# Kernel optimization log

Measured on AMD Instinct MI355X. Metric: run time of the kernel, lower is better.

The kernel has to match this reference:

```python
import jax, jax.numpy as jnp
import numpy as np

B, S, D, H = 2, 2048, 1024, 16
HD = D // H  # head_dim = 64
SCALE = 1.0 / np.sqrt(np.float32(D))  # original divides by sqrt(d_keys) == sqrt(d_model)


def setup_inputs() -> dict:
    key = jax.random.key(0)
    ks = jax.random.split(key, 8)
    inp = {
        "query": jax.random.normal(ks[0], (B, S, D), jnp.float32),
        "key": jax.random.normal(ks[1], (B, S, D), jnp.float32),
        "value": jax.random.normal(ks[2], (B, S, D), jnp.float32),
        # nn.Linear weights stored as [out, in]; y = x @ W.T
        "Wq": jax.random.normal(ks[3], (D, D), jnp.float32) * 0.02,
        "Wk": jax.random.normal(ks[4], (D, D), jnp.float32) * 0.02,
        "Wv": jax.random.normal(ks[5], (D, D), jnp.float32) * 0.02,
        "Wo": jax.random.normal(ks[6], (D, D), jnp.float32) * 0.02,
        "bo": jax.random.normal(ks[7], (D,), jnp.float32) * 0.02,
    }
    return inp


def reference(query, key, value, Wq, Wk, Wv, Wo, bo):
    # projections (no bias)
    Q = jnp.einsum('bsd,ed->bse', query, Wq)
    K = jnp.einsum('bsd,ed->bse', key, Wk)
    V = jnp.einsum('bsd,ed->bse', value, Wv)
    # split heads -> [B, H, S, HD]
    Q = Q.reshape(B, S, H, HD).transpose(0, 2, 1, 3)
    K = K.reshape(B, S, H, HD).transpose(0, 2, 1, 3)
    V = V.reshape(B, S, H, HD).transpose(0, 2, 1, 3)
    # scores [B,H,S,S]; note: scaled by 1/sqrt(d_model), matching the source
    scores = jnp.einsum('bhqd,bhkd->bhqk', Q, K) * SCALE
    attn = jax.nn.softmax(scores, axis=-1)  # dropout_ratio=0 -> identity
    ctx = jnp.einsum('bhqk,bhkd->bhqd', attn, V)
    ctx = ctx.transpose(0, 2, 1, 3).reshape(B, S, D)
    return jnp.einsum('bsd,ed->bse', ctx, Wo) + bo
```

## Files before the change

### kernel.cpp

```cpp
#include <hip/hip_runtime.h>
#include <hip/hip_bf16.h>

#define B_  2
#define S_  2048
#define D_  1024
#define H_  16
#define HD_ 64
#define SCALE_ 0.03125f
#define LOG2E_ 1.4426950408889634f
#define QSCALE_ (SCALE_ * LOG2E_)

typedef __bf16 bf16;
typedef __attribute__((ext_vector_type(8))) __bf16 bf16x8;
typedef __attribute__((ext_vector_type(8))) unsigned short u16x8;
typedef __attribute__((ext_vector_type(4))) __bf16 bf16x4;
typedef __attribute__((ext_vector_type(4))) float f32x4;

__device__ __forceinline__ void gload_lds16(const void* g, void* l) {
  __builtin_amdgcn_global_load_lds(
      (const __attribute__((address_space(1))) unsigned int*)g,
      (__attribute__((address_space(3))) unsigned int*)l,
      16, 0, 0);
}

__device__ __forceinline__ bf16x8 load8(const float* p) {
  const float4 a = *(const float4*)p;
  const float4 b = *(const float4*)(p + 4);
  bf16x8 r;
  r[0] = (bf16)a.x; r[1] = (bf16)a.y; r[2] = (bf16)a.z; r[3] = (bf16)a.w;
  r[4] = (bf16)b.x; r[5] = (bf16)b.y; r[6] = (bf16)b.z; r[7] = (bf16)b.w;
  return r;
}
__device__ __forceinline__ bf16x8 load8(const bf16* p) {
  return *(const bf16x8*)p;
}

__global__ __launch_bounds__(256)
void wconv_kernel(const float* __restrict__ Wq, const float* __restrict__ Wk,
                  const float* __restrict__ Wv, const float* __restrict__ Wo,
                  bf16* __restrict__ dst)
{
  const int n4  = (blockIdx.x * 256 + threadIdx.x) * 4;
  const int m   = n4 >> 20;
  const int off = n4 & ((1 << 20) - 1);
  const float* src = m == 0 ? Wq : (m == 1 ? Wk : (m == 2 ? Wv : Wo));
  const float4 a = *(const float4*)(src + off);
  bf16x4 o = {(bf16)a.x, (bf16)a.y, (bf16)a.z, (bf16)a.w};
  *(bf16x4*)(dst + n4) = o;
}

__global__ __launch_bounds__(256)
void conv_kernel(const float* __restrict__ Wq, const float* __restrict__ Wk,
                 const float* __restrict__ Wv, const float* __restrict__ Wo,
                 const float* __restrict__ q, const float* __restrict__ k,
                 const float* __restrict__ v, bf16* __restrict__ dst)
{
  const size_t MI = (size_t)1 << 20;
  const size_t n4 = ((size_t)blockIdx.x * 256 + threadIdx.x) * 4;
  const float* src;
  size_t so, dof;
  if (n4 < 4 * MI) {
    const int m = (int)(n4 >> 20);
    src = m == 0 ? Wq : (m == 1 ? Wk : (m == 2 ? Wv : Wo));
    so  = n4 & (MI - 1);
    dof = n4;
  } else {
    const size_t a = n4 - 4 * MI;
    const int m = (int)(a >> 22);
    src = m == 0 ? q : (m == 1 ? k : v);
    so  = a & (4 * MI - 1);
    dof = n4 + 4 * MI;
  }
  const float4 a4 = *(const float4*)(src + so);
  bf16x4 o = {(bf16)a4.x, (bf16)a4.y, (bf16)a4.z, (bf16)a4.w};
  *(bf16x4*)(dst + dof) = o;
}

__global__ __launch_bounds__(256, 2)
void gemm_qkv3_kernel(const bf16* __restrict__ Ab, const bf16* __restrict__ Wb,
                      bf16* __restrict__ Cq, bf16* __restrict__ Ck,
                      bf16* __restrict__ Cv)
{
  __shared__ bf16 lA[128 * 32];
  __shared__ bf16 lB[128 * 32];

  const int sel = blockIdx.y >> 3;
  const int bn  = blockIdx.y & 7;
  const bf16* A  = Ab + ((size_t)sel << 22);
  const bf16* Bw = Wb + ((size_t)sel << 20);
  bf16*       C  = sel == 0 ? Cq : (sel == 1 ? Ck : Cv);
  const float scale = sel == 0 ? QSCALE_ : 1.0f;

  const int t    = threadIdx.x;
  const int wave = t >> 6;
  const int lane = t & 63;
  const int quad = lane >> 4;
  const int l16  = lane & 15;
  const int bm = blockIdx.x;
  const int wm = (wave >> 1) * 64;
  const int wn = (wave & 1) * 64;

  const int srow = t >> 2;
  const int scol = (t & 3) * 8;
  const bf16* gA = A  + (size_t)(bm * 128 + srow) * D_ + scol;
  const bf16* gB = Bw + (size_t)(bn * 128 + srow) * D_ + scol;

  f32x4 acc[4][4] = {};

  for (int k0 = 0; k0 < D_; k0 += 32) {
    __syncthreads();
    gload_lds16(gA,                   (char*)lA + wave * 1024);
    gload_lds16(gA + (size_t)64 * D_, (char*)lA + 4096 + wave * 1024);
    gload_lds16(gB,                   (char*)lB + wave * 1024);
    gload_lds16(gB + (size_t)64 * D_, (char*)lB + 4096 + wave * 1024);
    __syncthreads();

    bf16x8 af[4], bfr[4];
#pragma unroll
    for (int i = 0; i < 4; ++i) {
      af[i]  = *(const bf16x8*)(lA + (wm + i * 16 + l16) * 32 + quad * 8);
      bfr[i] = *(const bf16x8*)(lB + (wn + i * 16 + l16) * 32 + quad * 8);
    }
#pragma unroll
    for (int mi = 0; mi < 4; ++mi)
#pragma unroll
      for (int ni = 0; ni < 4; ++ni)
        acc[mi][ni] = __builtin_amdgcn_mfma_f32_16x16x32_bf16(
            af[mi], bfr[ni], acc[mi][ni], 0, 0, 0);

    gA += 32;
    gB += 32;
  }

#pragma unroll
  for (int mi = 0; mi < 4; ++mi) {
#pragma unroll
    for (int ni = 0; ni < 4; ++ni) {
      const int col = bn * 128 + wn + ni * 16 + l16;
#pragma unroll
      for (int r = 0; r < 4; ++r) {
        const int row = bm * 128 + wm + mi * 16 + quad * 4 + r;
        C[(size_t)row * D_ + col] = (bf16)(acc[mi][ni][r] * scale);
      }
    }
  }
}

__global__ __launch_bounds__(256, 2)
void gemm_qkv_b_kernel(const float* __restrict__ Aq, const float* __restrict__ Ak,
                       const float* __restrict__ Av, const bf16* __restrict__ Wb,
                       bf16* __restrict__ Cq, bf16* __restrict__ Ck,
                       bf16* __restrict__ Cv)
{
  __shared__ bf16 lA[128 * 32];
  __shared__ bf16 lB[128 * 32];

  const int sel = blockIdx.y >> 3;
  const int bn  = blockIdx.y & 7;
  const float* A  = sel == 0 ? Aq : (sel == 1 ? Ak : Av);
  const bf16*  Bw = Wb + ((size_t)sel << 20);
  bf16*        C  = sel == 0 ? Cq : (sel == 1 ? Ck : Cv);
  const float scale = sel == 0 ? QSCALE_ : 1.0f;

  const int t    = threadIdx.x;
  const int wave = t >> 6;
  const int lane = t & 63;
  const int quad = lane >> 4;
  const int l16  = lane & 15;
  const int bm = blockIdx.x;
  const int wm = (wave >> 1) * 64;
  const int wn = (wave & 1) * 64;

  const int srow = t >> 2;
  const int scol = (t & 3) * 8;
  const float* gA  = A  + (size_t)(bm * 128 + srow) * D_ + scol;
  const bf16*  gBb = Bw + (size_t)(bn * 128 + srow) * D_ + scol;

  f32x4 acc[4][4] = {};

  bf16x8 a0 = load8(gA);
  bf16x8 a1 = load8(gA + (size_t)64 * D_);

  for (int k0 = 0; k0 < D_; k0 += 32) {
    __syncthreads();
    *(bf16x8*)(lA + srow * 32 + scol)        = a0;
    *(bf16x8*)(lA + (srow + 64) * 32 + scol) = a1;
    gload_lds16(gBb,                   (char*)lB + wave * 1024);
    gload_lds16(gBb + (size_t)64 * D_, (char*)lB + 4096 + wave * 1024);
    gBb += 32;
    __syncthreads();

    if (k0 + 32 < D_) {
      gA += 32;
      a0 = load8(gA);
      a1 = load8(gA + (size_t)64 * D_);
    }

    bf16x8 af[4], bfr[4];
#pragma unroll
    for (int i = 0; i < 4; ++i) {
      af[i]  = *(const bf16x8*)(lA + (wm + i * 16 + l16) * 32 + quad * 8);
      bfr[i] = *(const bf16x8*)(lB + (wn + i * 16 + l16) * 32 + quad * 8);
    }
#pragma unroll
    for (int mi = 0; mi < 4; ++mi)
#pragma unroll
      for (int ni = 0; ni < 4; ++ni)
        acc[mi][ni] = __builtin_amdgcn_mfma_f32_16x16x32_bf16(
            af[mi], bfr[ni], acc[mi][ni], 0, 0, 0);
  }

#pragma unroll
  for (int mi = 0; mi < 4; ++mi) {
#pragma unroll
    for (int ni = 0; ni < 4; ++ni) {
      const int col = bn * 128 + wn + ni * 16 + l16;
#pragma unroll
      for (int r = 0; r < 4; ++r) {
        const int row = bm * 128 + wm + mi * 16 + quad * 4 + r;
        C[(size_t)row * D_ + col] = (bf16)(acc[mi][ni][r] * scale);
      }
    }
  }
}

__global__ __launch_bounds__(256, 2)
void gemm_out_b_kernel(const bf16* __restrict__ A, const bf16* __restrict__ Bw,
                       const float* __restrict__ bias, float* __restrict__ C)
{
  __shared__ bf16 lA[128 * 32];
  __shared__ bf16 lB[64 * 32];

  const int t    = threadIdx.x;
  const int wave = t >> 6;
  const int lane = t & 63;
  const int quad = lane >> 4;
  const int l16  = lane & 15;
  const int bm = blockIdx.x;
  const int bn = blockIdx.y;
  const int wm = wave * 32;

  const int srow = t >> 2;
  const int scol = (t & 3) * 8;
  const bf16* gA = A  + (size_t)(bm * 128 + srow) * D_ + scol;
  const bf16* gB = Bw + (size_t)(bn * 64 + srow) * D_ + scol;

  f32x4 acc[2][4] = {};

  for (int k0 = 0; k0 < D_; k0 += 32) {
    __syncthreads();
    gload_lds16(gA,                   (char*)lA + wave * 1024);
    gload_lds16(gA + (size_t)64 * D_, (char*)lA + 4096 + wave * 1024);
    gload_lds16(gB,                   (char*)lB + wave * 1024);
    __syncthreads();

    bf16x8 af[2], bfr[4];
#pragma unroll
    for (int i = 0; i < 2; ++i)
      af[i]  = *(const bf16x8*)(lA + (wm + i * 16 + l16) * 32 + quad * 8);
#pragma unroll
    for (int i = 0; i < 4; ++i)
      bfr[i] = *(const bf16x8*)(lB + (i * 16 + l16) * 32 + quad * 8);
#pragma unroll
    for (int mi = 0; mi < 2; ++mi)
#pragma unroll
      for (int ni = 0; ni < 4; ++ni)
        acc[mi][ni] = __builtin_amdgcn_mfma_f32_16x16x32_bf16(
            af[mi], bfr[ni], acc[mi][ni], 0, 0, 0);

    gA += 32;
    gB += 32;
  }

  float bv[4];
#pragma unroll
  for (int ni = 0; ni < 4; ++ni)
    bv[ni] = bias[bn * 64 + ni * 16 + l16];
#pragma unroll
  for (int mi = 0; mi < 2; ++mi) {
#pragma unroll
    for (int ni = 0; ni < 4; ++ni) {
      const int col = bn * 64 + ni * 16 + l16;
#pragma unroll
      for (int r = 0; r < 4; ++r) {
        const int row = bm * 128 + wm + mi * 16 + quad * 4 + r;
        C[(size_t)row * D_ + col] = acc[mi][ni][r] + bv[ni];
      }
    }
  }
}

__global__ __launch_bounds__(256, 2)
void gemm_qkv_kernel(const float* __restrict__ Aq, const float* __restrict__ Ak,
                     const float* __restrict__ Av, const float* __restrict__ Wq,
                     const float* __restrict__ Wk, const float* __restrict__ Wv,
                     bf16* __restrict__ Cq, bf16* __restrict__ Ck,
                     bf16* __restrict__ Cv)
{
  __shared__ bf16 lA[128 * 32];
  __shared__ bf16 lB[128 * 32];

  const int sel = blockIdx.y >> 3;
  const int bn  = blockIdx.y & 7;
  const float* A  = sel == 0 ? Aq : (sel == 1 ? Ak : Av);
  const float* Bw = sel == 0 ? Wq : (sel == 1 ? Wk : Wv);
  bf16*        C  = sel == 0 ? Cq : (sel == 1 ? Ck : Cv);
  const float scale = sel == 0 ? QSCALE_ : 1.0f;

  const int t    = threadIdx.x;
  const int wave = t >> 6;
  const int lane = t & 63;
  const int quad = lane >> 4;
  const int l16  = lane & 15;
  const int bm = blockIdx.x;
  const int wm = (wave >> 1) * 64;
  const int wn = (wave & 1) * 64;

  const int srow = t >> 2;
  const int scol = (t & 3) * 8;
  const float* gA = A  + (size_t)(bm * 128 + srow) * D_ + scol;
  const float* gB = Bw + (size_t)(bn * 128 + srow) * D_ + scol;

  f32x4 acc[4][4] = {};

  for (int k0 = 0; k0 < D_; k0 += 32) {
    const bf16x8 a0 = load8(gA);
    const bf16x8 a1 = load8(gA + (size_t)64 * D_);
    const bf16x8 b0 = load8(gB);
    const bf16x8 b1 = load8(gB + (size_t)64 * D_);

    __syncthreads();
    *(bf16x8*)(lA + srow * 32 + scol)        = a0;
    *(bf16x8*)(lA + (srow + 64) * 32 + scol) = a1;
    *(bf16x8*)(lB + srow * 32 + scol)        = b0;
    *(bf16x8*)(lB + (srow + 64) * 32 + scol) = b1;
    __syncthreads();

    bf16x8 af[4], bfr[4];
#pragma unroll
    for (int i = 0; i < 4; ++i) {
      af[i]  = *(const bf16x8*)(lA + (wm + i * 16 + l16) * 32 + quad * 8);
      bfr[i] = *(const bf16x8*)(lB + (wn + i * 16 + l16) * 32 + quad * 8);
    }
#pragma unroll
    for (int mi = 0; mi < 4; ++mi)
#pragma unroll
      for (int ni = 0; ni < 4; ++ni)
        acc[mi][ni] = __builtin_amdgcn_mfma_f32_16x16x32_bf16(
            af[mi], bfr[ni], acc[mi][ni], 0, 0, 0);

    gA += 32;
    gB += 32;
  }

#pragma unroll
  for (int mi = 0; mi < 4; ++mi) {
#pragma unroll
    for (int ni = 0; ni < 4; ++ni) {
      const int col = bn * 128 + wn + ni * 16 + l16;
#pragma unroll
      for (int r = 0; r < 4; ++r) {
        const int row = bm * 128 + wm + mi * 16 + quad * 4 + r;
        C[(size_t)row * D_ + col] = (bf16)(acc[mi][ni][r] * scale);
      }
    }
  }
}

__global__ __launch_bounds__(256, 2)
void gemm_out_kernel(const bf16* __restrict__ A, const float* __restrict__ Bw,
                     const float* __restrict__ bias, float* __restrict__ C)
{
  __shared__ bf16 lA[128 * 32];
  __shared__ bf16 lB[64 * 32];

  const int t    = threadIdx.x;
  const int wave = t >> 6;
  const int lane = t & 63;
  const int quad = lane >> 4;
  const int l16  = lane & 15;
  const int bm = blockIdx.x;
  const int bn = blockIdx.y;
  const int wm = wave * 32;

  const int srow = t >> 2;
  const int scol = (t & 3) * 8;
  const bf16*  gA = A  + (size_t)(bm * 128 + srow) * D_ + scol;
  const float* gB = Bw + (size_t)(bn * 64 + srow) * D_ + scol;

  f32x4 acc[2][4] = {};

  for (int k0 = 0; k0 < D_; k0 += 32) {
    const bf16x8 a0 = load8(gA);
    const bf16x8 a1 = load8(gA + (size_t)64 * D_);
    const bf16x8 b0 = load8(gB);

    __syncthreads();
    *(bf16x8*)(lA + srow * 32 + scol)        = a0;
    *(bf16x8*)(lA + (srow + 64) * 32 + scol) = a1;
    *(bf16x8*)(lB + srow * 32 + scol)        = b0;
    __syncthreads();

    bf16x8 af[2], bfr[4];
#pragma unroll
    for (int i = 0; i < 2; ++i)
      af[i]  = *(const bf16x8*)(lA + (wm + i * 16 + l16) * 32 + quad * 8);
#pragma unroll
    for (int i = 0; i < 4; ++i)
      bfr[i] = *(const bf16x8*)(lB + (i * 16 + l16) * 32 + quad * 8);
#pragma unroll
    for (int mi = 0; mi < 2; ++mi)
#pragma unroll
      for (int ni = 0; ni < 4; ++ni)
        acc[mi][ni] = __builtin_amdgcn_mfma_f32_16x16x32_bf16(
            af[mi], bfr[ni], acc[mi][ni], 0, 0, 0);

    gA += 32;
    gB += 32;
  }

  float bv[4];
#pragma unroll
  for (int ni = 0; ni < 4; ++ni)
    bv[ni] = bias[bn * 64 + ni * 16 + l16];
#pragma unroll
  for (int mi = 0; mi < 2; ++mi) {
#pragma unroll
    for (int ni = 0; ni < 4; ++ni) {
      const int col = bn * 64 + ni * 16 + l16;
#pragma unroll
      for (int r = 0; r < 4; ++r) {
        const int row = bm * 128 + wm + mi * 16 + quad * 4 + r;
        C[(size_t)row * D_ + col] = acc[mi][ni][r] + bv[ni];
      }
    }
  }
}

__global__ __launch_bounds__(256, 2)
void attn_kernel(const bf16* Q, const bf16* __restrict__ K,
                 const bf16* __restrict__ V, bf16* O)
{
  __shared__ bf16 lQ[128 * 72];
  __shared__ bf16 lK[64 * 72];
  __shared__ bf16 lVT[64 * 72];
  __shared__ bf16 lP[4][32 * 72];

  const int t    = threadIdx.x;
  const int wave = t >> 6;
  const int lane = t & 63;
  const int quad = lane >> 4;
  const int l16  = lane & 15;

  const int flat = blockIdx.y * 16 + blockIdx.x;
  const int qt   = (flat >> 3) & 15;
  const int bh   = (flat & 7) * 4 + (flat >> 7);
  const size_t headoff =
      (size_t)(bh >> 4) * ((size_t)S_ * D_) + (size_t)(bh & 15) * HD_;

  const int sr  = t >> 3;
  const int scx = (t & 7) * 8;
#pragma unroll
  for (int i = 0; i < 4; ++i) {
    const bf16x8 qv =
        *(const bf16x8*)(Q + headoff + (size_t)(qt * 128 + sr + 32 * i) * D_ + scx);
    *(bf16x8*)(lQ + (sr + 32 * i) * 72 + scx) = qv;
  }
  __syncthreads();

  bf16x8 qf[2][2];
#pragma unroll
  for (int m = 0; m < 2; ++m)
#pragma unroll
    for (int ks = 0; ks < 2; ++ks)
      qf[m][ks] = *(const bf16x8*)(lQ + (wave * 32 + m * 16 + l16) * 72 +
                                   (ks * 4 + quad) * 8);

  f32x4 acco[2][4] = {};
  float den[2] = {0.f, 0.f};

  const int dp = t & 31;
  const int kg = t >> 5;

  bf16x8 pk0, pk1;
  unsigned int pv[8];
  {
    const bf16* kb = K + headoff + (size_t)sr * D_ + scx;
    pk0 = load8(kb);
    pk1 = load8(kb + (size_t)32 * D_);
    const bf16* vb = V + headoff + (size_t)(kg * 8) * D_ + 2 * dp;
#pragma unroll
    for (int j = 0; j < 8; ++j)
      pv[j] = *(const unsigned int*)(vb + (size_t)j * D_);
  }

  for (int kt = 0; kt < S_ / 64; ++kt) {
    __syncthreads();

    *(bf16x8*)(lK + sr * 72 + scx)        = pk0;
    *(bf16x8*)(lK + (sr + 32) * 72 + scx) = pk1;
    {
      u16x8 w0, w1;
#pragma unroll
      for (int j = 0; j < 8; ++j) {
        w0[j] = (unsigned short)(pv[j] & 0xffffu);
        w1[j] = (unsigned short)(pv[j] >> 16);
      }
      *(u16x8*)(lVT + (2 * dp) * 72 + kg * 8)     = w0;
      *(u16x8*)(lVT + (2 * dp + 1) * 72 + kg * 8) = w1;
    }
    __syncthreads();

    if (kt + 1 < S_ / 64) {
      const bf16* kb = K + headoff + (size_t)((kt + 1) * 64 + sr) * D_ + scx;
      pk0 = load8(kb);
      pk1 = load8(kb + (size_t)32 * D_);
      const bf16* vb = V + headoff + (size_t)((kt + 1) * 64 + kg * 8) * D_ + 2 * dp;
#pragma unroll
      for (int j = 0; j < 8; ++j)
        pv[j] = *(const unsigned int*)(vb + (size_t)j * D_);
    }

    f32x4 sc[2][4] = {};
#pragma unroll
    for (int nt = 0; nt < 4; ++nt) {
#pragma unroll
      for (int ks = 0; ks < 2; ++ks) {
        const bf16x8 kf =
            *(const bf16x8*)(lK + (nt * 16 + l16) * 72 + (ks * 4 + quad) * 8);
#pragma unroll
        for (int m = 0; m < 2; ++m)
          sc[m][nt] = __builtin_amdgcn_mfma_f32_16x16x32_bf16(
              kf, qf[m][ks], sc[m][nt], 0, 0, 0);
      }
    }

    bf16* lPw = lP[wave];
#pragma unroll
    for (int m = 0; m < 2; ++m) {
#pragma unroll
      for (int nt = 0; nt < 4; ++nt) {
        bf16x4 pw;
#pragma unroll
        for (int r = 0; r < 4; ++r) {
          const float p = __builtin_amdgcn_exp2f(sc[m][nt][r]);
          pw[r] = (bf16)p;
          den[m] += p;
        }
        *(bf16x4*)(lPw + (m * 16 + l16) * 72 + nt * 16 + quad * 4) = pw;
      }
    }

    __syncthreads();

    bf16x8 pf[2][2];
#pragma unroll
    for (int m = 0; m < 2; ++m)
#pragma unroll
      for (int ks = 0; ks < 2; ++ks)
        pf[m][ks] = *(const bf16x8*)(lPw + (m * 16 + l16) * 72 +
                                     ks * 32 + quad * 8);
#pragma unroll
    for (int dt = 0; dt < 4; ++dt) {
#pragma unroll
      for (int ks = 0; ks < 2; ++ks) {
        const bf16x8 vf =
            *(const bf16x8*)(lVT + (dt * 16 + l16) * 72 + (ks * 4 + quad) * 8);
#pragma unroll
        for (int m = 0; m < 2; ++m)
          acco[m][dt] = __builtin_amdgcn_mfma_f32_16x16x32_bf16(
              pf[m][ks], vf, acco[m][dt], 0, 0, 0);
      }
    }
  }

#pragma unroll
  for (int m = 0; m < 2; ++m) {
    den[m] += __shfl_xor(den[m], 16);
    den[m] += __shfl_xor(den[m], 32);
  }
#pragma unroll
  for (int m = 0; m < 2; ++m) {
#pragma unroll
    for (int r = 0; r < 4; ++r) {
      const float rd  = 1.f / __shfl(den[m], quad * 4 + r);
      const int   row = qt * 128 + wave * 32 + m * 16 + quad * 4 + r;
#pragma unroll
      for (int dt = 0; dt < 4; ++dt)
        O[headoff + (size_t)row * D_ + dt * 16 + l16] =
            (bf16)(acco[m][dt][r] * rd);
    }
  }
}

extern "C" void kernel_launch(void* const* d_in, const int* in_sizes, int n_in,
                              void* d_out, int out_size, void* d_ws, size_t ws_size,
                              hipStream_t stream)
{
  const float* q  = (const float*)d_in[0];
  const float* k  = (const float*)d_in[1];
  const float* v  = (const float*)d_in[2];
  const float* Wq = (const float*)d_in[3];
  const float* Wk = (const float*)d_in[4];
  const float* Wv = (const float*)d_in[5];
  const float* Wo = (const float*)d_in[6];
  const float* bo = (const float*)d_in[7];
  float* outf = (float*)d_out;
  bf16*  outs = (bf16*)d_out;
  bf16*  wsb  = (bf16*)d_ws;

  const size_t MD = (size_t)B_ * S_ * D_;

  dim3 blk(256);
  dim3 gqkv(B_ * S_ / 128, 24);
  dim3 gattn(S_ / 128, B_ * H_);
  dim3 gout(B_ * S_ / 128, D_ / 64);

  bf16* Kp = outs;
  bf16* Vp = outs + MD;

  if (ws_size >= (size_t)40 << 20) {
    bf16* Wb = wsb;
    bf16* Qp = wsb + MD;
    bf16* Ab = wsb + 2 * MD;

    conv_kernel<<<16384, blk, 0, stream>>>(Wq, Wk, Wv, Wo, q, k, v, wsb);
    gemm_qkv3_kernel<<<gqkv, blk, 0, stream>>>(Ab, Wb, Qp, Kp, Vp);
    attn_kernel<<<gattn, blk, 0, stream>>>(Qp, Kp, Vp, Qp);
    gemm_out_b_kernel<<<gout, blk, 0, stream>>>(Qp, Wb + 3 * ((size_t)1 << 20),
                                                bo, outf);
  } else if (ws_size >= (size_t)16 << 20) {
    bf16* Wb = wsb;
    bf16* Qp = wsb + MD;

    wconv_kernel<<<4096, blk, 0, stream>>>(Wq, Wk, Wv, Wo, Wb);
    gemm_qkv_b_kernel<<<gqkv, blk, 0, stream>>>(q, k, v, Wb, Qp, Kp, Vp);
    attn_kernel<<<gattn, blk, 0, stream>>>(Qp, Kp, Vp, Qp);
    gemm_out_b_kernel<<<gout, blk, 0, stream>>>(Qp, Wb + 3 * ((size_t)1 << 20),
                                                bo, outf);
  } else {
    bf16* Qp = wsb;

    gemm_qkv_kernel<<<gqkv, blk, 0, stream>>>(q, k, v, Wq, Wk, Wv,
                                              Qp, Kp, Vp);
    attn_kernel<<<gattn, blk, 0, stream>>>(Qp, Kp, Vp, Qp);
    gemm_out_kernel<<<gout, blk, 0, stream>>>(Qp, Wo, bo, outf);
  }
}
```

Baseline: 211.5 us.

## Double-buffer K/V tiles in LDS and cut attention-loop barriers to one

The attention kernel now keeps two LDS buffers each for the K tile and the transposed V tile. Each iteration writes the next tile into the spare buffer while computing on the current one, and global prefetch now runs two tiles ahead. The barrier before the P·V stage becomes a compiler-only scheduling fence, because each wave reads only the P buffer it wrote itself. That leaves a single __syncthreads per iteration instead of three. The cost is more LDS per block and one extra prefetch stage held in registers, which could reduce occupancy.

New measurement: 213.1 us. Within noise of the previous version (+0.8%).

```diff
diff --git a/kernel.cpp b/kernel.cpp
--- a/kernel.cpp
+++ b/kernel.cpp
@@ -442,8 +442,8 @@
                  const bf16* __restrict__ V, bf16* O)
 {
   __shared__ bf16 lQ[128 * 72];
-  __shared__ bf16 lK[64 * 72];
-  __shared__ bf16 lVT[64 * 72];
+  __shared__ bf16 lK[2][64 * 72];
+  __shared__ bf16 lVT[2][64 * 72];
   __shared__ bf16 lP[4][32 * 72];
 
   const int t    = threadIdx.x;
@@ -458,6 +458,9 @@
   const size_t headoff =
       (size_t)(bh >> 4) * ((size_t)S_ * D_) + (size_t)(bh & 15) * HD_;
 
+  const bf16* Kb = K + headoff;
+  const bf16* Vb = V + headoff;
+
   const int sr  = t >> 3;
   const int scx = (t & 7) * 8;
 #pragma unroll
@@ -482,40 +485,67 @@
   const int dp = t & 31;
   const int kg = t >> 5;
 
+  const int NT = S_ / 64;
   bf16x8 pk0, pk1;
   unsigned int pv[8];
+
   {
-    const bf16* kb = K + headoff + (size_t)sr * D_ + scx;
+    const bf16* kb = Kb + (size_t)sr * D_ + scx;
     pk0 = load8(kb);
     pk1 = load8(kb + (size_t)32 * D_);
-    const bf16* vb = V + headoff + (size_t)(kg * 8) * D_ + 2 * dp;
+    const bf16* vb = Vb + (size_t)(kg * 8) * D_ + 2 * dp;
 #pragma unroll
     for (int j = 0; j < 8; ++j)
       pv[j] = *(const unsigned int*)(vb + (size_t)j * D_);
   }
-
-  for (int kt = 0; kt < S_ / 64; ++kt) {
-    __syncthreads();
-
-    *(bf16x8*)(lK + sr * 72 + scx)        = pk0;
-    *(bf16x8*)(lK + (sr + 32) * 72 + scx) = pk1;
-    {
+  {
+    *(bf16x8*)(lK[0] + sr * 72 + scx)        = pk0;
+    *(bf16x8*)(lK[0] + (sr + 32) * 72 + scx) = pk1;
+    u16x8 w0, w1;
+#pragma unroll
+    for (int j = 0; j < 8; ++j) {
+      w0[j] = (unsigned short)(pv[j] & 0xffffu);
+      w1[j] = (unsigned short)(pv[j] >> 16);
+    }
+    *(u16x8*)(lVT[0] + (2 * dp) * 72 + kg * 8)     = w0;
+    *(u16x8*)(lVT[0] + (2 * dp + 1) * 72 + kg * 8) = w1;
+  }
+  {
+    const bf16* kb = Kb + (size_t)(64 + sr) * D_ + scx;
+    pk0 = load8(kb);
+    pk1 = load8(kb + (size_t)32 * D_);
+    const bf16* vb = Vb + (size_t)(64 + kg * 8) * D_ + 2 * dp;
+#pragma unroll
+    for (int j = 0; j < 8; ++j)
+      pv[j] = *(const unsigned int*)(vb + (size_t)j * D_);
+  }
+  __syncthreads();
+
+  for (int kt = 0; kt < NT; ++kt) {
+    const int cur = kt & 1;
+    bf16* lKc  = lK[cur];
+    bf16* lVc  = lVT[cur];
+
+    if (kt + 1 < NT) {
+      bf16* lKn = lK[cur ^ 1];
+      bf16* lVn = lVT[cur ^ 1];
+      *(bf16x8*)(lKn + sr * 72 + scx)        = pk0;
+      *(bf16x8*)(lKn + (sr + 32) * 72 + scx) = pk1;
       u16x8 w0, w1;
 #pragma unroll
       for (int j = 0; j < 8; ++j) {
         w0[j] = (unsigned short)(pv[j] & 0xffffu);
         w1[j] = (unsigned short)(pv[j] >> 16);
       }
-      *(u16x8*)(lVT + (2 * dp) * 72 + kg * 8)     = w0;
-      *(u16x8*)(lVT + (2 * dp + 1) * 72 + kg * 8) = w1;
-    }
-    __syncthreads();
-
-    if (kt + 1 < S_ / 64) {
-      const bf16* kb = K + headoff + (size_t)((kt + 1) * 64 + sr) * D_ + scx;
+      *(u16x8*)(lVn + (2 * dp) * 72 + kg * 8)     = w0;
+      *(u16x8*)(lVn + (2 * dp + 1) * 72 + kg * 8) = w1;
+    }
+
+    if (kt + 2 < NT) {
+      const bf16* kb = Kb + (size_t)((kt + 2) * 64 + sr) * D_ + scx;
       pk0 = load8(kb);
       pk1 = load8(kb + (size_t)32 * D_);
-      const bf16* vb = V + headoff + (size_t)((kt + 1) * 64 + kg * 8) * D_ + 2 * dp;
+      const bf16* vb = Vb + (size_t)((kt + 2) * 64 + kg * 8) * D_ + 2 * dp;
 #pragma unroll
       for (int j = 0; j < 8; ++j)
         pv[j] = *(const unsigned int*)(vb + (size_t)j * D_);
@@ -527,7 +557,7 @@
 #pragma unroll
       for (int ks = 0; ks < 2; ++ks) {
         const bf16x8 kf =
-            *(const bf16x8*)(lK + (nt * 16 + l16) * 72 + (ks * 4 + quad) * 8);
+            *(const bf16x8*)(lKc + (nt * 16 + l16) * 72 + (ks * 4 + quad) * 8);
 #pragma unroll
         for (int m = 0; m < 2; ++m)
           sc[m][nt] = __builtin_amdgcn_mfma_f32_16x16x32_bf16(
@@ -551,7 +581,8 @@
       }
     }
 
-    __syncthreads();
+    asm volatile("" ::: "memory");
+    __builtin_amdgcn_sched_barrier(0);
 
     bf16x8 pf[2][2];
 #pragma unroll
@@ -565,13 +596,15 @@
 #pragma unroll
       for (int ks = 0; ks < 2; ++ks) {
         const bf16x8 vf =
-            *(const bf16x8*)(lVT + (dt * 16 + l16) * 72 + (ks * 4 + quad) * 8);
+            *(const bf16x8*)(lVc + (dt * 16 + l16) * 72 + (ks * 4 + quad) * 8);
 #pragma unroll
         for (int m = 0; m < 2; ++m)
           acco[m][dt] = __builtin_amdgcn_mfma_f32_16x16x32_bf16(
               pf[m][ks], vf, acco[m][dt], 0, 0, 0);
       }
     }
+
+    __syncthreads();
   }
 
 #pragma unroll
```
